# Kernel tuning notes

Measured on AMD Instinct MI355X. Metric: run time of the kernel, lower is better.

## Reference

```python
import jax, jax.numpy as jnp
import numpy as np

IMG = 8       # image_size
LH = 150      # l_h
LQ = 10       # l_q
K = 10        # value-iteration steps
B = 16384     # batch
N_STATES = 2 + IMG * IMG


def _conv(x, w, pad):
    # NCHW conv, stride 1
    return jax.lax.conv_general_dilated(
        x, w, window_strides=(1, 1), padding=[(pad, pad), (pad, pad)],
        dimension_numbers=('NCHW', 'OIHW', 'NCHW'))


def setup_inputs() -> dict:
    key = jax.random.key(0)
    ks = jax.random.split(key, 8)
    grid = jax.random.normal(ks[0], (B, IMG * IMG), dtype=jnp.float32)
    pos = jax.random.randint(ks[1], (B, 2), 0, IMG).astype(jnp.float32)
    S = jnp.concatenate([grid, pos], axis=1)                      # [B, 66]
    Wh = jax.random.normal(ks[2], (LH, 1, 3, 3), jnp.float32) * 0.1
    bh = jnp.zeros((LH,), jnp.float32)
    Wr = jax.random.normal(ks[3], (1, LH, 1, 1), jnp.float32) * 0.1
    Wq = jax.random.normal(ks[4], (LQ, 1, 3, 3), jnp.float32) * 0.1
    w = jax.random.normal(ks[5], (LQ, 1, 3, 3), jnp.float32) * 0.1
    Wfc = jax.random.normal(ks[6], (8, LQ), jnp.float32) * 0.1
    return {'S': S, 'Wh': Wh, 'bh': bh, 'Wr': Wr, 'Wq': Wq, 'w': w, 'Wfc': Wfc}


def reference(S, Wh, bh, Wr, Wq, w, Wfc):
    X = S[:, :IMG * IMG].reshape(-1, 1, IMG, IMG)                 # [B,1,8,8]
    s1 = S[:, IMG * IMG].astype(jnp.int32)                        # row index
    s2 = S[:, IMG * IMG + 1].astype(jnp.int32)                    # col index

    h = _conv(X, Wh, 1) + bh[None, :, None, None]                 # [B,150,8,8]
    r = _conv(h, Wr, 0)                                           # [B,1,8,8]
    q = _conv(r, Wq, 1)                                           # [B,10,8,8]
    v = jnp.max(q, axis=1, keepdims=True)                         # [B,1,8,8]

    Wcat = jnp.concatenate([Wq, w], axis=1)                       # [10,2,3,3]

    def step(v, _):
        qq = _conv(jnp.concatenate([r, v], axis=1), Wcat, 1)
        return jnp.max(qq, axis=1, keepdims=True), None

    v, _ = jax.lax.scan(step, v, None, length=K - 1)
    q = _conv(jnp.concatenate([r, v], axis=1), Wcat, 1)           # [B,10,8,8]

    bidx = jnp.arange(q.shape[0])
    q_sel = q[bidx, :, s1, s2]                                    # [B,10]
    logits = q_sel @ Wfc.T                                        # [B,8]
    return logits
```

## Files before the change

kernel.cpp:

```cpp
#include <hip/hip_runtime.h>

#define IMG 8
#define LH 150
#define LQ 10
#define KITER 10
#define ROW (IMG * IMG + 2)

__device__ __forceinline__ float bperm(int byte_addr, float v) {
    return __builtin_bit_cast(float,
        __builtin_amdgcn_ds_bpermute(byte_addr, __builtin_bit_cast(int, v)));
}

__device__ __forceinline__ float max10(const float q[LQ]) {
    const float g0 = fmaxf(fmaxf(q[0], q[1]), q[2]);
    const float g1 = fmaxf(fmaxf(q[3], q[4]), q[5]);
    const float g2 = fmaxf(fmaxf(q[6], q[7]), q[8]);
    return fmaxf(fmaxf(g0, g1), fmaxf(g2, q[9]));
}

__global__ void weff_kernel(const float* __restrict__ Wh,
                            const float* __restrict__ bh,
                            const float* __restrict__ Wr,
                            float* __restrict__ ws) {
    const int wv = threadIdx.x >> 6;
    const int lane = threadIdx.x & 63;
    float partial = 0.f;
    for (int c = lane; c < LH; c += 64) {
        const float wr = Wr[c];
        partial += wr * ((wv < 9) ? Wh[c * 9 + wv] : bh[c]);
    }
    #pragma unroll
    for (int off = 32; off > 0; off >>= 1)
        partial += __shfl_xor(partial, off);
    if (lane == 0) ws[wv] = partial;
}

__global__ __launch_bounds__(256) void vin_kernel(
    const float* __restrict__ S,
    const float* __restrict__ Wq,
    const float* __restrict__ w,
    const float* __restrict__ Wfc,
    const float* __restrict__ ws,
    float* __restrict__ out,
    int B) {
    const int wave = threadIdx.x >> 6;
    const int lane = threadIdx.x & 63;
    const long b0 = (long)(blockIdx.x * 4 + wave) * 2;
    if (b0 >= B) return;

    const int y = lane >> 3, x = lane & 7;

    int   addr[9];
    float msk[9];
    #pragma unroll
    for (int t = 0; t < 9; ++t) {
        const int dy = t / 3 - 1, dx = t % 3 - 1;
        const int ny = y + dy, nx = x + dx;
        const bool v = ((unsigned)ny < 8u) && ((unsigned)nx < 8u);
        addr[t] = (v ? (ny * 8 + nx) : 0) << 2;
        msk[t]  = v ? 1.f : 0.f;
    }

    const float* S0 = S + b0 * ROW;
    const float X0 = S0[lane];
    const float X1 = S0[ROW + lane];
    const int sel0 = (int)S0[IMG * IMG] * 8 + (int)S0[IMG * IMG + 1];
    const int sel1 = (int)S0[ROW + IMG * IMG] * 8 + (int)S0[ROW + IMG * IMG + 1];

    float r0 = ws[9], r1 = ws[9];
    #pragma unroll
    for (int t = 0; t < 9; ++t) {
        const float wm = ws[t] * msk[t];
        r0 = fmaf(wm, bperm(addr[t], X0), r0);
        r1 = fmaf(wm, bperm(addr[t], X1), r1);
    }

    float qr0[LQ], qr1[LQ];
    #pragma unroll
    for (int t = 0; t < 9; ++t) {
        const float a0 = bperm(addr[t], r0) * msk[t];
        const float a1 = bperm(addr[t], r1) * msk[t];
        #pragma unroll
        for (int o = 0; o < LQ; ++o) {
            const float wq = Wq[o * 9 + t];
            if (t == 0) { qr0[o] = a0 * wq; qr1[o] = a1 * wq; }
            else        { qr0[o] = fmaf(a0, wq, qr0[o]);
                          qr1[o] = fmaf(a1, wq, qr1[o]); }
        }
    }

    float v0 = max10(qr0), v1 = max10(qr1);

    float q0[LQ], q1[LQ];
    #pragma unroll
    for (int k = 0; k < KITER; ++k) {
        #pragma unroll
        for (int t = 0; t < 9; ++t) {
            const float a0 = bperm(addr[t], v0) * msk[t];
            const float a1 = bperm(addr[t], v1) * msk[t];
            #pragma unroll
            for (int o = 0; o < LQ; ++o) {
                const float wt = w[o * 9 + t];
                if (t == 0) { q0[o] = fmaf(a0, wt, qr0[o]);
                              q1[o] = fmaf(a1, wt, qr1[o]); }
                else        { q0[o] = fmaf(a0, wt, q0[o]);
                              q1[o] = fmaf(a1, wt, q1[o]); }
            }
        }
        v0 = max10(q0);
        v1 = max10(q1);
    }

    float qs0[LQ], qs1[LQ];
    #pragma unroll
    for (int o = 0; o < LQ; ++o) {
        qs0[o] = bperm(sel0 << 2, q0[o]);
        qs1[o] = bperm(sel1 << 2, q1[o]);
    }

    if (lane < 16) {
        const int row = lane & 7;
        float acc = 0.f;
        #pragma unroll
        for (int o = 0; o < LQ; ++o)
            acc = fmaf((lane < 8) ? qs0[o] : qs1[o], Wfc[row * LQ + o], acc);
        out[b0 * 8 + lane] = acc;
    }
}

extern "C" void kernel_launch(void* const* d_in, const int* in_sizes, int n_in,
                              void* d_out, int out_size, void* d_ws, size_t ws_size,
                              hipStream_t stream) {
    const float* S   = (const float*)d_in[0];
    const float* Wh  = (const float*)d_in[1];
    const float* bh  = (const float*)d_in[2];
    const float* Wr  = (const float*)d_in[3];
    const float* Wq  = (const float*)d_in[4];
    const float* w   = (const float*)d_in[5];
    const float* Wfc = (const float*)d_in[6];
    float* out = (float*)d_out;
    float* ws  = (float*)d_ws;

    const int B = in_sizes[0] / ROW;

    weff_kernel<<<1, 640, 0, stream>>>(Wh, bh, Wr, ws);

    const int grid = (B + 7) / 8;
    vin_kernel<<<grid, 256, 0, stream>>>(S, Wq, w, Wfc, ws, out, B);
}
```

Baseline: 101.4 us.

## Remap VIN kernel to 8 images per wave with DPP row shifts

Each wave now handles 8 batch elements, with each lane owning one image column and keeping all 8 rows in registers. The 3x3 stencil uses DPP row shifts for horizontal neighbours and register indexing for vertical ones, replacing the many ds_bpermute calls. Each lane computes one output logit, so the selection and FC stage fill the whole wave. The cost is much higher register pressure (qr[10][8] plus the v arrays), which the launch_bounds occupancy hint constrains, and the iteration loop is no longer unrolled.

```diff
diff --git a/kernel.cpp b/kernel.cpp
--- a/kernel.cpp
+++ b/kernel.cpp
@@ -6,16 +6,18 @@
 #define KITER 10
 #define ROW (IMG * IMG + 2)
 
+#define DPP_ROW_SHR1 0x111
+#define DPP_ROW_SHL1 0x101
+template <int CTRL>
+__device__ __forceinline__ float dppf(float v) {
+    return __builtin_bit_cast(float,
+        __builtin_amdgcn_update_dpp(0, __builtin_bit_cast(int, v),
+                                    CTRL, 0xF, 0xF, true));
+}
+
 __device__ __forceinline__ float bperm(int byte_addr, float v) {
     return __builtin_bit_cast(float,
         __builtin_amdgcn_ds_bpermute(byte_addr, __builtin_bit_cast(int, v)));
-}
-
-__device__ __forceinline__ float max10(const float q[LQ]) {
-    const float g0 = fmaxf(fmaxf(q[0], q[1]), q[2]);
-    const float g1 = fmaxf(fmaxf(q[3], q[4]), q[5]);
-    const float g2 = fmaxf(fmaxf(q[6], q[7]), q[8]);
-    return fmaxf(fmaxf(g0, g1), fmaxf(g2, q[9]));
 }
 
 __global__ void weff_kernel(const float* __restrict__ Wh,
@@ -35,7 +37,7 @@
     if (lane == 0) ws[wv] = partial;
 }
 
-__global__ __launch_bounds__(256) void vin_kernel(
+__global__ __launch_bounds__(256, 2) void vin_kernel(
     const float* __restrict__ S,
     const float* __restrict__ Wq,
     const float* __restrict__ w,
@@ -45,87 +47,146 @@
     int B) {
     const int wave = threadIdx.x >> 6;
     const int lane = threadIdx.x & 63;
-    const long b0 = (long)(blockIdx.x * 4 + wave) * 2;
-    if (b0 >= B) return;
-
-    const int y = lane >> 3, x = lane & 7;
-
-    int   addr[9];
-    float msk[9];
-    #pragma unroll
-    for (int t = 0; t < 9; ++t) {
-        const int dy = t / 3 - 1, dx = t % 3 - 1;
-        const int ny = y + dy, nx = x + dx;
-        const bool v = ((unsigned)ny < 8u) && ((unsigned)nx < 8u);
-        addr[t] = (v ? (ny * 8 + nx) : 0) << 2;
-        msk[t]  = v ? 1.f : 0.f;
-    }
-
-    const float* S0 = S + b0 * ROW;
-    const float X0 = S0[lane];
-    const float X1 = S0[ROW + lane];
-    const int sel0 = (int)S0[IMG * IMG] * 8 + (int)S0[IMG * IMG + 1];
-    const int sel1 = (int)S0[ROW + IMG * IMG] * 8 + (int)S0[ROW + IMG * IMG + 1];
-
-    float r0 = ws[9], r1 = ws[9];
-    #pragma unroll
-    for (int t = 0; t < 9; ++t) {
-        const float wm = ws[t] * msk[t];
-        r0 = fmaf(wm, bperm(addr[t], X0), r0);
-        r1 = fmaf(wm, bperm(addr[t], X1), r1);
-    }
-
-    float qr0[LQ], qr1[LQ];
-    #pragma unroll
-    for (int t = 0; t < 9; ++t) {
-        const float a0 = bperm(addr[t], r0) * msk[t];
-        const float a1 = bperm(addr[t], r1) * msk[t];
+    const long wid = (long)blockIdx.x * 4 + wave;
+    if (wid * 8 >= B) return;
+
+    const int x = lane & 7;
+    const int irow = (lane >> 3) * ROW;
+    const float mskL = (x == 0) ? 0.f : 1.f;
+    const float mskR = (x == 7) ? 0.f : 1.f;
+
+    const float* Sw = S + wid * 8 * ROW;
+
+    float X[8];
+    #pragma unroll
+    for (int y = 0; y < 8; ++y) X[y] = Sw[irow + y * 8 + x];
+    const int s1 = (int)Sw[irow + 64];
+    const int s2 = (int)Sw[irow + 65];
+    const int selb = ((lane & 56) + s2) << 2;
+
+    float XL[8], XR[8];
+    #pragma unroll
+    for (int y = 0; y < 8; ++y) {
+        XL[y] = dppf<DPP_ROW_SHR1>(X[y]) * mskL;
+        XR[y] = dppf<DPP_ROW_SHL1>(X[y]) * mskR;
+    }
+    float r[8];
+    #pragma unroll
+    for (int y = 0; y < 8; ++y) {
+        float acc = ws[9];
+        #pragma unroll
+        for (int t = 0; t < 9; ++t) {
+            const int dy = t / 3 - 1, dx = t % 3 - 1;
+            const int yy = y + dy;
+            if (yy < 0 || yy > 7) continue;
+            const float val = (dx < 0) ? XL[yy] : ((dx > 0) ? XR[yy] : X[yy]);
+            acc = fmaf(ws[t], val, acc);
+        }
+        r[y] = acc;
+    }
+
+    float rL[8], rR[8];
+    #pragma unroll
+    for (int y = 0; y < 8; ++y) {
+        rL[y] = dppf<DPP_ROW_SHR1>(r[y]) * mskL;
+        rR[y] = dppf<DPP_ROW_SHL1>(r[y]) * mskR;
+    }
+    float qr[LQ][8];
+    #pragma unroll
+    for (int o = 0; o < LQ; ++o) {
+        #pragma unroll
+        for (int y = 0; y < 8; ++y) {
+            float acc = 0.f;
+            #pragma unroll
+            for (int t = 0; t < 9; ++t) {
+                const int dy = t / 3 - 1, dx = t % 3 - 1;
+                const int yy = y + dy;
+                if (yy < 0 || yy > 7) continue;
+                const float val = (dx < 0) ? rL[yy] : ((dx > 0) ? rR[yy] : r[yy]);
+                acc = fmaf(val, Wq[o * 9 + t], acc);
+            }
+            qr[o][y] = acc;
+        }
+    }
+
+    float v[8];
+    #pragma unroll
+    for (int y = 0; y < 8; ++y) {
+        float m = qr[0][y];
+        #pragma unroll
+        for (int o = 1; o < LQ; ++o) m = fmaxf(m, qr[o][y]);
+        v[y] = m;
+    }
+
+    #pragma unroll 1
+    for (int k = 0; k < KITER - 1; ++k) {
+        float vL[8], vR[8];
+        #pragma unroll
+        for (int y = 0; y < 8; ++y) {
+            vL[y] = dppf<DPP_ROW_SHR1>(v[y]) * mskL;
+            vR[y] = dppf<DPP_ROW_SHL1>(v[y]) * mskR;
+        }
+        float m[8];
         #pragma unroll
         for (int o = 0; o < LQ; ++o) {
-            const float wq = Wq[o * 9 + t];
-            if (t == 0) { qr0[o] = a0 * wq; qr1[o] = a1 * wq; }
-            else        { qr0[o] = fmaf(a0, wq, qr0[o]);
-                          qr1[o] = fmaf(a1, wq, qr1[o]); }
-        }
-    }
-
-    float v0 = max10(qr0), v1 = max10(qr1);
-
-    float q0[LQ], q1[LQ];
-    #pragma unroll
-    for (int k = 0; k < KITER; ++k) {
-        #pragma unroll
-        for (int t = 0; t < 9; ++t) {
-            const float a0 = bperm(addr[t], v0) * msk[t];
-            const float a1 = bperm(addr[t], v1) * msk[t];
             #pragma unroll
-            for (int o = 0; o < LQ; ++o) {
-                const float wt = w[o * 9 + t];
-                if (t == 0) { q0[o] = fmaf(a0, wt, qr0[o]);
-                              q1[o] = fmaf(a1, wt, qr1[o]); }
-                else        { q0[o] = fmaf(a0, wt, q0[o]);
-                              q1[o] = fmaf(a1, wt, q1[o]); }
+            for (int y = 0; y < 8; ++y) {
+                float acc = qr[o][y];
+                #pragma unroll
+                for (int t = 0; t < 9; ++t) {
+                    const int dy = t / 3 - 1, dx = t % 3 - 1;
+                    const int yy = y + dy;
+                    if (yy < 0 || yy > 7) continue;
+                    const float val = (dx < 0) ? vL[yy] : ((dx > 0) ? vR[yy] : v[yy]);
+                    acc = fmaf(val, w[o * 9 + t], acc);
+                }
+                m[y] = (o == 0) ? acc : fmaxf(m[y], acc);
             }
         }
-        v0 = max10(q0);
-        v1 = max10(q1);
-    }
-
-    float qs0[LQ], qs1[LQ];
+        #pragma unroll
+        for (int y = 0; y < 8; ++y) v[y] = m[y];
+    }
+
+    float wfc[LQ];
+    #pragma unroll
+    for (int o = 0; o < LQ; ++o) wfc[o] = Wfc[x * LQ + o];
+
+    float vL[8], vR[8];
+    #pragma unroll
+    for (int y = 0; y < 8; ++y) {
+        vL[y] = dppf<DPP_ROW_SHR1>(v[y]) * mskL;
+        vR[y] = dppf<DPP_ROW_SHL1>(v[y]) * mskR;
+    }
+    const bool sb0 = (s1 & 1) != 0, sb1 = (s1 & 2) != 0, sb2 = (s1 & 4) != 0;
+    float logit = 0.f;
     #pragma unroll
     for (int o = 0; o < LQ; ++o) {
-        qs0[o] = bperm(sel0 << 2, q0[o]);
-        qs1[o] = bperm(sel1 << 2, q1[o]);
-    }
-
-    if (lane < 16) {
-        const int row = lane & 7;
-        float acc = 0.f;
-        #pragma unroll
-        for (int o = 0; o < LQ; ++o)
-            acc = fmaf((lane < 8) ? qs0[o] : qs1[o], Wfc[row * LQ + o], acc);
-        out[b0 * 8 + lane] = acc;
-    }
+        float q[8];
+        #pragma unroll
+        for (int y = 0; y < 8; ++y) {
+            float acc = qr[o][y];
+            #pragma unroll
+            for (int t = 0; t < 9; ++t) {
+                const int dy = t / 3 - 1, dx = t % 3 - 1;
+                const int yy = y + dy;
+                if (yy < 0 || yy > 7) continue;
+                const float val = (dx < 0) ? vL[yy] : ((dx > 0) ? vR[yy] : v[yy]);
+                acc = fmaf(val, w[o * 9 + t], acc);
+            }
+            q[y] = acc;
+        }
+        const float a0 = sb0 ? q[1] : q[0];
+        const float a1 = sb0 ? q[3] : q[2];
+        const float a2 = sb0 ? q[5] : q[4];
+        const float a3 = sb0 ? q[7] : q[6];
+        const float c0 = sb1 ? a1 : a0;
+        const float c1 = sb1 ? a3 : a2;
+        const float qy = sb2 ? c1 : c0;
+        const float qsel = bperm(selb, qy);
+        logit = fmaf(qsel, wfc[o], logit);
+    }
+
+    out[wid * 64 + lane] = logit;
 }
 
 extern "C" void kernel_launch(void* const* d_in, const int* in_sizes, int n_in,
@@ -145,6 +206,6 @@
 
     weff_kernel<<<1, 640, 0, stream>>>(Wh, bh, Wr, ws);
 
-    const int grid = (B + 7) / 8;
+    const int grid = (B + 31) / 32;
     vin_kernel<<<grid, 256, 0, stream>>>(S, Wq, w, Wfc, ws, out, B);
 }
```

Measured after the change: 97.16 us. 1.04x faster.

## Remap VIN stencil to 4 images per wave with DPP row shifts

Applied to the files above, without the earlier changes.

Each wave now holds 4 images, with each lane owning 4 rows of a column pair-half layout. The 3x3 stencil neighbours come from DPP row/lane shifts instead of nine ds_bpermute calls per convolution, which removes LDS-crossbar permute traffic from the value-iteration loop. The final Q selection uses a per-lane row select followed by a single bpermute. The value-iteration loop is no longer unrolled and launch bounds request 4 blocks per CU. The risks are higher register pressure from holding qr[10][4], and correctness depends on DPP row-shift semantics at the 16-lane row boundaries matching the chosen lane layout.

```diff
diff --git a/kernel.cpp b/kernel.cpp
--- a/kernel.cpp
+++ b/kernel.cpp
@@ -6,16 +6,20 @@
 #define KITER 10
 #define ROW (IMG * IMG + 2)
 
+#define DPP_SHR1 0x111
+#define DPP_SHL1 0x101
+#define DPP_SHR8 0x118
+#define DPP_SHL8 0x108
+template <int CTRL>
+__device__ __forceinline__ float dppf(float v) {
+    return __builtin_bit_cast(float,
+        __builtin_amdgcn_update_dpp(0, __builtin_bit_cast(int, v),
+                                    CTRL, 0xF, 0xF, true));
+}
+
 __device__ __forceinline__ float bperm(int byte_addr, float v) {
     return __builtin_bit_cast(float,
         __builtin_amdgcn_ds_bpermute(byte_addr, __builtin_bit_cast(int, v)));
-}
-
-__device__ __forceinline__ float max10(const float q[LQ]) {
-    const float g0 = fmaxf(fmaxf(q[0], q[1]), q[2]);
-    const float g1 = fmaxf(fmaxf(q[3], q[4]), q[5]);
-    const float g2 = fmaxf(fmaxf(q[6], q[7]), q[8]);
-    return fmaxf(fmaxf(g0, g1), fmaxf(g2, q[9]));
 }
 
 __global__ void weff_kernel(const float* __restrict__ Wh,
@@ -35,7 +39,7 @@
     if (lane == 0) ws[wv] = partial;
 }
 
-__global__ __launch_bounds__(256) void vin_kernel(
+__global__ __launch_bounds__(256, 4) void vin_kernel(
     const float* __restrict__ S,
     const float* __restrict__ Wq,
     const float* __restrict__ w,
@@ -45,87 +49,106 @@
     int B) {
     const int wave = threadIdx.x >> 6;
     const int lane = threadIdx.x & 63;
-    const long b0 = (long)(blockIdx.x * 4 + wave) * 2;
-    if (b0 >= B) return;
+    const long wid = (long)blockIdx.x * 4 + wave;
+    if (wid * 4 >= B) return;
 
-    const int y = lane >> 3, x = lane & 7;
+    const int x = lane & 7;
+    const int ioff = (lane >> 4) * ROW;
+    const float mskL = (x == 0) ? 0.f : 1.f;
+    const float mskR = (x == 7) ? 0.f : 1.f;
 
-    int   addr[9];
-    float msk[9];
+    const float* Sb = S + wid * 4 * ROW;
+    const int ybase = ((lane >> 3) & 1) * 32 + x;
+
+    float X[4];
     #pragma unroll
-    for (int t = 0; t < 9; ++t) {
-        const int dy = t / 3 - 1, dx = t % 3 - 1;
-        const int ny = y + dy, nx = x + dx;
-        const bool v = ((unsigned)ny < 8u) && ((unsigned)nx < 8u);
-        addr[t] = (v ? (ny * 8 + nx) : 0) << 2;
-        msk[t]  = v ? 1.f : 0.f;
+    for (int yy = 0; yy < 4; ++yy) X[yy] = Sb[ioff + ybase + yy * 8];
+    const int s1 = (int)Sb[ioff + 64];
+    const int s2 = (int)Sb[ioff + 65];
+
+    float C[6], L[6], R[6];
+    auto expand = [&](const float V[4]) {
+        C[0] = dppf<DPP_SHR8>(V[3]);
+        C[1] = V[0]; C[2] = V[1]; C[3] = V[2]; C[4] = V[3];
+        C[5] = dppf<DPP_SHL8>(V[0]);
+        #pragma unroll
+        for (int j = 0; j < 6; ++j) {
+            L[j] = dppf<DPP_SHR1>(C[j]) * mskL;
+            R[j] = dppf<DPP_SHL1>(C[j]) * mskR;
+        }
+    };
+    auto conv9 = [&](int yy, const float* wt, float acc) {
+        acc = fmaf(L[yy],     wt[0], acc);
+        acc = fmaf(C[yy],     wt[1], acc);
+        acc = fmaf(R[yy],     wt[2], acc);
+        acc = fmaf(L[yy + 1], wt[3], acc);
+        acc = fmaf(C[yy + 1], wt[4], acc);
+        acc = fmaf(R[yy + 1], wt[5], acc);
+        acc = fmaf(L[yy + 2], wt[6], acc);
+        acc = fmaf(C[yy + 2], wt[7], acc);
+        acc = fmaf(R[yy + 2], wt[8], acc);
+        return acc;
+    };
+
+    expand(X);
+    float r[4];
+    #pragma unroll
+    for (int yy = 0; yy < 4; ++yy) r[yy] = conv9(yy, ws, ws[9]);
+
+    expand(r);
+    float qr[LQ][4];
+    #pragma unroll
+    for (int o = 0; o < LQ; ++o)
+        #pragma unroll
+        for (int yy = 0; yy < 4; ++yy)
+            qr[o][yy] = conv9(yy, Wq + o * 9, 0.f);
+
+    float v[4];
+    #pragma unroll
+    for (int yy = 0; yy < 4; ++yy) {
+        float m = qr[0][yy];
+        #pragma unroll
+        for (int o = 1; o < LQ; ++o) m = fmaxf(m, qr[o][yy]);
+        v[yy] = m;
     }
 
-    const float* S0 = S + b0 * ROW;
-    const float X0 = S0[lane];
-    const float X1 = S0[ROW + lane];
-    const int sel0 = (int)S0[IMG * IMG] * 8 + (int)S0[IMG * IMG + 1];
-    const int sel1 = (int)S0[ROW + IMG * IMG] * 8 + (int)S0[ROW + IMG * IMG + 1];
-
-    float r0 = ws[9], r1 = ws[9];
-    #pragma unroll
-    for (int t = 0; t < 9; ++t) {
-        const float wm = ws[t] * msk[t];
-        r0 = fmaf(wm, bperm(addr[t], X0), r0);
-        r1 = fmaf(wm, bperm(addr[t], X1), r1);
+    #pragma unroll 1
+    for (int k = 0; k < KITER - 1; ++k) {
+        expand(v);
+        float m[4];
+        #pragma unroll
+        for (int o = 0; o < LQ; ++o) {
+            #pragma unroll
+            for (int yy = 0; yy < 4; ++yy) {
+                const float acc = conv9(yy, w + o * 9, qr[o][yy]);
+                m[yy] = (o == 0) ? acc : fmaxf(m[yy], acc);
+            }
+        }
+        #pragma unroll
+        for (int yy = 0; yy < 4; ++yy) v[yy] = m[yy];
     }
 
-    float qr0[LQ], qr1[LQ];
+    float wfc[LQ];
     #pragma unroll
-    for (int t = 0; t < 9; ++t) {
-        const float a0 = bperm(addr[t], r0) * msk[t];
-        const float a1 = bperm(addr[t], r1) * msk[t];
+    for (int o = 0; o < LQ; ++o) wfc[o] = Wfc[x * LQ + o];
+
+    expand(v);
+    const bool sb0 = (s1 & 1) != 0, sb1 = (s1 & 2) != 0;
+    const int selb = ((lane & 48) + (s1 >> 2) * 8 + s2) << 2;
+    float logit = 0.f;
+    #pragma unroll
+    for (int o = 0; o < LQ; ++o) {
+        float q[4];
         #pragma unroll
-        for (int o = 0; o < LQ; ++o) {
-            const float wq = Wq[o * 9 + t];
-            if (t == 0) { qr0[o] = a0 * wq; qr1[o] = a1 * wq; }
-            else        { qr0[o] = fmaf(a0, wq, qr0[o]);
-                          qr1[o] = fmaf(a1, wq, qr1[o]); }
-        }
+        for (int yy = 0; yy < 4; ++yy) q[yy] = conv9(yy, w + o * 9, qr[o][yy]);
+        const float t0 = sb0 ? q[1] : q[0];
+        const float t1 = sb0 ? q[3] : q[2];
+        const float qy = sb1 ? t1 : t0;
+        logit = fmaf(bperm(selb, qy), wfc[o], logit);
     }
 
-    float v0 = max10(qr0), v1 = max10(qr1);
-
-    float q0[LQ], q1[LQ];
-    #pragma unroll
-    for (int k = 0; k < KITER; ++k) {
-        #pragma unroll
-        for (int t = 0; t < 9; ++t) {
-            const float a0 = bperm(addr[t], v0) * msk[t];
-            const float a1 = bperm(addr[t], v1) * msk[t];
-            #pragma unroll
-            for (int o = 0; o < LQ; ++o) {
-                const float wt = w[o * 9 + t];
-                if (t == 0) { q0[o] = fmaf(a0, wt, qr0[o]);
-                              q1[o] = fmaf(a1, wt, qr1[o]); }
-                else        { q0[o] = fmaf(a0, wt, q0[o]);
-                              q1[o] = fmaf(a1, wt, q1[o]); }
-            }
-        }
-        v0 = max10(q0);
-        v1 = max10(q1);
-    }
-
-    float qs0[LQ], qs1[LQ];
-    #pragma unroll
-    for (int o = 0; o < LQ; ++o) {
-        qs0[o] = bperm(sel0 << 2, q0[o]);
-        qs1[o] = bperm(sel1 << 2, q1[o]);
-    }
-
-    if (lane < 16) {
-        const int row = lane & 7;
-        float acc = 0.f;
-        #pragma unroll
-        for (int o = 0; o < LQ; ++o)
-            acc = fmaf((lane < 8) ? qs0[o] : qs1[o], Wfc[row * LQ + o], acc);
-        out[b0 * 8 + lane] = acc;
-    }
+    if ((lane & 8) == 0)
+        out[wid * 32 + (lane >> 4) * 8 + x] = logit;
 }
 
 extern "C" void kernel_launch(void* const* d_in, const int* in_sizes, int n_in,
@@ -145,6 +168,6 @@
 
     weff_kernel<<<1, 640, 0, stream>>>(Wh, bh, Wr, ws);
 
-    const int grid = (B + 7) / 8;
+    const int grid = (B + 15) / 16;
     vin_kernel<<<grid, 256, 0, stream>>>(S, Wq, w, Wfc, ws, out, B);
 }
```

Result: faster. 98.92 us (-2.4%).
